# Optimization experiments

Measured on AMD Instinct MI355X. Metric: run time of the kernel, lower is better.

The kernel has to match this reference:

```python
import jax, jax.numpy as jnp
import numpy as np

H = 16
D_MODEL = 1024
D_K = D_MODEL // H
B, S = 8, 1024


def setup_inputs() -> dict:
    key = jax.random.key(0)
    ks = jax.random.split(key, 11)
    scale = 1.0 / np.sqrt(D_MODEL)
    inp = {
        "query": jax.random.normal(ks[0], (B, S, D_MODEL), jnp.float32),
        "key_": jax.random.normal(ks[1], (B, S, D_MODEL), jnp.float32),
        "value": jax.random.normal(ks[2], (B, S, D_MODEL), jnp.float32),
        "w_q": jax.random.normal(ks[3], (D_MODEL, D_MODEL), jnp.float32) * scale,
        "b_q": jnp.zeros((D_MODEL,), jnp.float32),
        "w_k": jax.random.normal(ks[4], (D_MODEL, D_MODEL), jnp.float32) * scale,
        "b_k": jnp.zeros((D_MODEL,), jnp.float32),
        "w_v": jax.random.normal(ks[5], (D_MODEL, D_MODEL), jnp.float32) * scale,
        "b_v": jnp.zeros((D_MODEL,), jnp.float32),
        "w_o": jax.random.normal(ks[6], (D_MODEL, D_MODEL), jnp.float32) * scale,
        "b_o": jnp.zeros((D_MODEL,), jnp.float32),
    }
    return inp


def reference(query, key_, value, w_q, b_q, w_k, b_k, w_v, b_v, w_o, b_o):
    # Linear projections (torch Linear: x @ W.T + b), then split heads: [B,S,D] -> [B,H,S,d_k]
    def proj(x, w, b):
        y = jnp.einsum("bsd,ed->bse", x, w) + b
        return y.reshape(B, S, H, D_K).transpose(0, 2, 1, 3)

    q = proj(query, w_q, b_q)
    k = proj(key_, w_k, b_k)
    v = proj(value, w_v, b_v)

    # Scaled dot-product attention (mask=None, dropout p=0 -> identity)
    scores = jnp.einsum("bhqd,bhkd->bhqk", q, k) / jnp.sqrt(jnp.float32(D_K))
    attn = jax.nn.softmax(scores, axis=-1)
    ctx = jnp.einsum("bhqk,bhkd->bhqd", attn, v)  # [B,H,S,d_k]

    # Merge heads and final output projection
    ctx = ctx.transpose(0, 2, 1, 3).reshape(B, S, D_MODEL)
    return jnp.einsum("bsd,ed->bse", ctx, w_o) + b_o
```

## Files before the change

kernel.cpp:

```cpp
#include <hip/hip_runtime.h>
#include <hip/hip_bf16.h>

#define NH 16
#define DK 64
#define BB 8
#define SS 1024
#define DM 1024
#define MTOT (BB * SS)

typedef float f4v __attribute__((ext_vector_type(4)));
typedef float f16v __attribute__((ext_vector_type(16)));
typedef short s16v8 __attribute__((ext_vector_type(8)));
typedef unsigned short u16v4 __attribute__((ext_vector_type(4)));
typedef unsigned short u16v8 __attribute__((ext_vector_type(8)));

#define EXP2F(x) __builtin_amdgcn_exp2f(x)

__device__ __forceinline__ unsigned short f2bf(float x) {
    unsigned int u = __float_as_uint(x);
    u += 0x7FFFu + ((u >> 16) & 1u);
    return (unsigned short)(u >> 16);
}

__device__ __forceinline__ unsigned int packbf2(float lo, float hi) {
    return ((unsigned int)f2bf(hi) << 16) | f2bf(lo);
}

__device__ __forceinline__ void gload16(const void* g, void* l) {
    __builtin_amdgcn_global_load_lds(
        (const __attribute__((address_space(1))) void*)g,
        (__attribute__((address_space(3))) void*)l, 16, 0, 0);
}

struct Src7 { const float* p[7]; };

__global__ __launch_bounds__(256) void cvt_all(Src7 sp, unsigned short* __restrict__ dst) {
    const size_t e = ((size_t)blockIdx.x * 256 + threadIdx.x) * 8;
    const int unit = (int)(e >> 20);
    int t; size_t base;
    if (unit < 8)       { t = 0; base = 0; }
    else if (unit < 16) { t = 1; base = (size_t)8 << 20; }
    else if (unit < 24) { t = 2; base = (size_t)16 << 20; }
    else                { t = 3 + (unit - 24); base = (size_t)unit << 20; }
    const float* s = sp.p[t] + (e - base);
    f4v a = *(const f4v*)s;
    f4v b = *(const f4v*)(s + 4);
    u16v8 o;
    o[0] = f2bf(a[0]); o[1] = f2bf(a[1]); o[2] = f2bf(a[2]); o[3] = f2bf(a[3]);
    o[4] = f2bf(b[0]); o[5] = f2bf(b[1]); o[6] = f2bf(b[2]); o[7] = f2bf(b[3]);
    *(u16v8*)(dst + e) = o;
}

struct QkvArgs {
    const unsigned short* X[3];
    const unsigned short* W[3];
    const float* bias[3];
    unsigned short* Y[3];
};

__global__ __launch_bounds__(256) void gemm_qkv(QkvArgs a) {
    __shared__ unsigned short As[128 * 32];
    __shared__ unsigned short Bs[128 * 32];
    const int z = blockIdx.z;
    const unsigned short* X = a.X[z];
    const unsigned short* W = a.W[z];
    const float* bias = a.bias[z];
    unsigned short* Y = a.Y[z];

    const int tid = threadIdx.x;
    const int wv = tid >> 6, l = tid & 63;
    const int lq = l & 15, g = l >> 4;
    const int wr = wv >> 1, wc = wv & 1;
    const int m0 = blockIdx.y * 128, n0 = blockIdx.x * 128;

    f4v acc[4][4];
#pragma unroll
    for (int i = 0; i < 4; ++i)
#pragma unroll
        for (int j = 0; j < 4; ++j) acc[i][j] = (f4v){0.f, 0.f, 0.f, 0.f};

    for (int kt = 0; kt < DM / 32; ++kt) {
        const int k0 = kt * 32;
        __syncthreads();
#pragma unroll
        for (int p = 0; p < 2; ++p) {
            const int u = p * 256 + tid;
            const int row = u >> 2, kc = u & 3;
            gload16(X + (size_t)(m0 + row) * DM + k0 + kc * 8, As + (size_t)u * 8);
            gload16(W + (size_t)(n0 + row) * DM + k0 + kc * 8, Bs + (size_t)u * 8);
        }
        __syncthreads();

        s16v8 av[4], bv[4];
#pragma unroll
        for (int i = 0; i < 4; ++i)
            av[i] = *(const s16v8*)(As + (wr * 64 + i * 16 + lq) * 32 + g * 8);
#pragma unroll
        for (int j = 0; j < 4; ++j)
            bv[j] = *(const s16v8*)(Bs + (wc * 64 + j * 16 + lq) * 32 + g * 8);
#pragma unroll
        for (int i = 0; i < 4; ++i)
#pragma unroll
            for (int j = 0; j < 4; ++j)
                acc[i][j] = __builtin_amdgcn_mfma_f32_16x16x32_bf16(av[i], bv[j], acc[i][j], 0, 0, 0);
    }

#pragma unroll
    for (int j = 0; j < 4; ++j) {
        const int col = n0 + wc * 64 + j * 16 + lq;
        const float bvl = bias[col];
#pragma unroll
        for (int i = 0; i < 4; ++i) {
            const int row0 = m0 + wr * 64 + i * 16 + g * 4;
            if (z < 2) {
#pragma unroll
                for (int r = 0; r < 4; ++r) {
                    const int row = row0 + r;
                    const int b_ = row >> 10, s_ = row & (SS - 1);
                    const int h_ = col >> 6, d_ = col & (DK - 1);
                    Y[((size_t)(b_ * NH + h_) * SS + s_) * DK + d_] = f2bf(acc[i][j][r] + bvl);
                }
            } else {
                const int b_ = row0 >> 10, s0_ = row0 & (SS - 1);
                const int h_ = col >> 6, d_ = col & (DK - 1);
                u16v4 o;
#pragma unroll
                for (int r = 0; r < 4; ++r) o[r] = f2bf(acc[i][j][r] + bvl);
                *(u16v4*)&Y[((size_t)(b_ * NH + h_) * DK + d_) * SS + s0_] = o;
            }
        }
    }
}

__global__ __launch_bounds__(256) void gemm_out(const unsigned short* __restrict__ X,
                                                const unsigned short* __restrict__ W,
                                                const float* __restrict__ bias,
                                                float* __restrict__ Y) {
    __shared__ unsigned short As[128 * 32];
    __shared__ unsigned short Bs[128 * 32];
    const int tid = threadIdx.x;
    const int wv = tid >> 6, l = tid & 63;
    const int lq = l & 15, g = l >> 4;
    const int wr = wv >> 1, wc = wv & 1;
    const int m0 = blockIdx.y * 128, n0 = blockIdx.x * 128;

    f4v acc[4][4];
#pragma unroll
    for (int i = 0; i < 4; ++i)
#pragma unroll
        for (int j = 0; j < 4; ++j) acc[i][j] = (f4v){0.f, 0.f, 0.f, 0.f};

    for (int kt = 0; kt < DM / 32; ++kt) {
        const int k0 = kt * 32;
        __syncthreads();
#pragma unroll
        for (int p = 0; p < 2; ++p) {
            const int u = p * 256 + tid;
            const int row = u >> 2, kc = u & 3;
            gload16(X + (size_t)(m0 + row) * DM + k0 + kc * 8, As + (size_t)u * 8);
            gload16(W + (size_t)(n0 + row) * DM + k0 + kc * 8, Bs + (size_t)u * 8);
        }
        __syncthreads();

        s16v8 av[4], bv[4];
#pragma unroll
        for (int i = 0; i < 4; ++i)
            av[i] = *(const s16v8*)(As + (wr * 64 + i * 16 + lq) * 32 + g * 8);
#pragma unroll
        for (int j = 0; j < 4; ++j)
            bv[j] = *(const s16v8*)(Bs + (wc * 64 + j * 16 + lq) * 32 + g * 8);
#pragma unroll
        for (int i = 0; i < 4; ++i)
#pragma unroll
            for (int j = 0; j < 4; ++j)
                acc[i][j] = __builtin_amdgcn_mfma_f32_16x16x32_bf16(av[i], bv[j], acc[i][j], 0, 0, 0);
    }

#pragma unroll
    for (int j = 0; j < 4; ++j) {
        const int col = n0 + wc * 64 + j * 16 + lq;
        const float bvl = bias[col];
#pragma unroll
        for (int i = 0; i < 4; ++i) {
#pragma unroll
            for (int r = 0; r < 4; ++r) {
                const int row = m0 + wr * 64 + i * 16 + g * 4 + r;
                Y[(size_t)row * DM + col] = acc[i][j][r] + bvl;
            }
        }
    }
}

__global__ __launch_bounds__(256) void attn_mfma32(const unsigned short* __restrict__ Qp,
                                                   const unsigned short* __restrict__ Kp,
                                                   const unsigned short* __restrict__ Vt,
                                                   unsigned short* __restrict__ ctx) {
    const int tid = threadIdx.x;
    const int wv = tid >> 6;
    const int l = tid & 63;
    const int l31 = l & 31, hi = l >> 5;
    const int bh = blockIdx.x;
    const int q = blockIdx.y * 128 + wv * 32 + l31;
    const float C = 0.18033688011112042f;

    const unsigned short* Qrow = Qp + ((size_t)bh * SS + q) * DK + hi * 8;
    s16v8 qf[4];
#pragma unroll
    for (int kd = 0; kd < 4; ++kd) qf[kd] = *(const s16v8*)(Qrow + kd * 16);

    const unsigned short* Kb = Kp + (size_t)bh * SS * DK + hi * 8;
    const unsigned short* Vb = Vt + (size_t)bh * DK * SS + hi * 8;

    f16v O0, O1;
#pragma unroll
    for (int r = 0; r < 16; ++r) { O0[r] = 0.f; O1[r] = 0.f; }
    float me = -1e30f;
    float lr = 0.f;

    for (int t = 0; t < SS / 64; ++t) {
        s16v8 kf[2][4];
#pragma unroll
        for (int ks = 0; ks < 2; ++ks)
#pragma unroll
            for (int kd = 0; kd < 4; ++kd)
                kf[ks][kd] = *(const s16v8*)(Kb + (size_t)(t * 64 + ks * 32 + l31) * DK + kd * 16);
        s16v8 vf[2][4];
#pragma unroll
        for (int db = 0; db < 2; ++db)
#pragma unroll
            for (int ksg = 0; ksg < 4; ++ksg)
                vf[db][ksg] = *(const s16v8*)(Vb + (size_t)(db * 32 + l31) * SS + t * 64 + ksg * 16);

        f16v s0, s1;
#pragma unroll
        for (int r = 0; r < 16; ++r) { s0[r] = 0.f; s1[r] = 0.f; }
#pragma unroll
        for (int kd = 0; kd < 4; ++kd) {
            s0 = __builtin_amdgcn_mfma_f32_32x32x16_bf16(kf[0][kd], qf[kd], s0, 0, 0, 0);
            s1 = __builtin_amdgcn_mfma_f32_32x32x16_bf16(kf[1][kd], qf[kd], s1, 0, 0, 0);
        }

        float mx = s0[0];
#pragma unroll
        for (int r = 1; r < 16; ++r) mx = fmaxf(mx, s0[r]);
#pragma unroll
        for (int r = 0; r < 16; ++r) mx = fmaxf(mx, s1[r]);
        mx = fmaxf(mx, __shfl_xor(mx, 32));
        const float mxl = mx * C;

        const bool need = !__all(mxl - me <= 8.0f);
        float corr = 1.0f;
        if (need) {
            const float mnew = fmaxf(me, mxl);
            corr = EXP2F(me - mnew);
            me = mnew;
        }

        float rs = 0.f;
#pragma unroll
        for (int r = 0; r < 16; ++r) { s0[r] = EXP2F(__fmaf_rn(s0[r], C, -me)); rs += s0[r]; }
#pragma unroll
        for (int r = 0; r < 16; ++r) { s1[r] = EXP2F(__fmaf_rn(s1[r], C, -me)); rs += s1[r]; }
        rs += __shfl_xor(rs, 32);
        if (need) {
            lr = lr * corr + rs;
#pragma unroll
            for (int r = 0; r < 16; ++r) { O0[r] *= corr; O1[r] *= corr; }
        } else {
            lr += rs;
        }

        s16v8 pb[2][2];
#pragma unroll
        for (int ks = 0; ks < 2; ++ks) {
            unsigned int u[8], su[8];
#pragma unroll
            for (int i = 0; i < 8; ++i) {
                const float plo = (ks == 0) ? s0[2 * i] : s1[2 * i];
                const float phi = (ks == 0) ? s0[2 * i + 1] : s1[2 * i + 1];
                u[i] = packbf2(plo, phi);
            }
#pragma unroll
            for (int i = 0; i < 8; ++i) su[i] = (unsigned int)__shfl_xor((int)u[i], 32);
#pragma unroll
            for (int kk = 0; kk < 2; ++kk) {
                const int base = 4 * kk + 2 * hi;
                union { unsigned int w[4]; s16v8 s; } f;
                f.w[0] = hi ? su[base] : u[base];
                f.w[1] = hi ? su[base + 1] : u[base + 1];
                f.w[2] = hi ? u[base] : su[base];
                f.w[3] = hi ? u[base + 1] : su[base + 1];
                pb[ks][kk] = f.s;
            }
        }

#pragma unroll
        for (int ksg = 0; ksg < 4; ++ksg) {
            O0 = __builtin_amdgcn_mfma_f32_32x32x16_bf16(vf[0][ksg], pb[ksg >> 1][ksg & 1], O0, 0, 0, 0);
            O1 = __builtin_amdgcn_mfma_f32_32x32x16_bf16(vf[1][ksg], pb[ksg >> 1][ksg & 1], O1, 0, 0, 0);
        }
    }

    const float inv = 1.0f / lr;
    const int b_ = bh >> 4, h_ = bh & 15;
    unsigned short* crow = ctx + ((size_t)b_ * SS + q) * DM + h_ * DK;
#pragma unroll
    for (int g2 = 0; g2 < 4; ++g2) {
        u16v4 o0, o1;
#pragma unroll
        for (int r2 = 0; r2 < 4; ++r2) {
            o0[r2] = f2bf(O0[4 * g2 + r2] * inv);
            o1[r2] = f2bf(O1[4 * g2 + r2] * inv);
        }
        *(u16v4*)(crow + 8 * g2 + 4 * hi) = o0;
        *(u16v4*)(crow + 32 + 8 * g2 + 4 * hi) = o1;
    }
}

extern "C" void kernel_launch(void* const* d_in, const int* in_sizes, int n_in,
                              void* d_out, int out_size, void* d_ws, size_t ws_size,
                              hipStream_t stream) {
    const float* query = (const float*)d_in[0];
    const float* key_  = (const float*)d_in[1];
    const float* value = (const float*)d_in[2];
    const float* w_q = (const float*)d_in[3];
    const float* b_q = (const float*)d_in[4];
    const float* w_k = (const float*)d_in[5];
    const float* b_k = (const float*)d_in[6];
    const float* w_v = (const float*)d_in[7];
    const float* b_v = (const float*)d_in[8];
    const float* w_o = (const float*)d_in[9];
    const float* b_o = (const float*)d_in[10];

    unsigned short* ws = (unsigned short*)d_ws;
    const size_t NX = (size_t)MTOT * DM;
    const size_t NW = (size_t)DM * DM;
    unsigned short* xq  = ws;
    unsigned short* xk  = xq + NX;
    unsigned short* xv  = xk + NX;
    unsigned short* wqb = xv + NX;
    unsigned short* wkb = wqb + NW;
    unsigned short* wvb = wkb + NW;
    unsigned short* wob = wvb + NW;
    unsigned short* Qp  = wob + NW;
    unsigned short* Kp  = Qp + NX;
    unsigned short* VpT = Kp + NX;
    unsigned short* ctx = xq;

    Src7 sp;
    sp.p[0] = query; sp.p[1] = key_; sp.p[2] = value;
    sp.p[3] = w_q; sp.p[4] = w_k; sp.p[5] = w_v; sp.p[6] = w_o;
    cvt_all<<<14336, 256, 0, stream>>>(sp, ws);

    QkvArgs qa;
    qa.X[0] = xq;  qa.X[1] = xk;  qa.X[2] = xv;
    qa.W[0] = wqb; qa.W[1] = wkb; qa.W[2] = wvb;
    qa.bias[0] = b_q; qa.bias[1] = b_k; qa.bias[2] = b_v;
    qa.Y[0] = Qp; qa.Y[1] = Kp; qa.Y[2] = VpT;
    gemm_qkv<<<dim3(DM / 128, MTOT / 128, 3), 256, 0, stream>>>(qa);

    attn_mfma32<<<dim3(BB * NH, SS / 128), 256, 0, stream>>>(Qp, Kp, VpT, ctx);

    gemm_out<<<dim3(DM / 128, MTOT / 128), 256, 0, stream>>>(ctx, wob, b_o, (float*)d_out);
}
```

Measured before the change: 441.0 us.

## Stage K/V tiles through double-buffered LDS via async global-to-LDS loads in attention

The attention kernel now copies each 64-key K tile and V^T tile into shared memory with global_load_lds, double-buffered so the next tile's load overlaps compute on the current one. Each tile is loaded once per workgroup and shared by its four waves, where before every wave read it from global memory itself. The grid is flattened to 1D with bh as the fast index, so workgroups sharing a head are scheduled close together. This adds barriers and a waitcnt per iteration, 32KB of LDS that may limit occupancy, and an extra redundant stage on the last iteration.

```diff
diff --git a/kernel.cpp b/kernel.cpp
--- a/kernel.cpp
+++ b/kernel.cpp
@@ -15,6 +15,7 @@
 typedef unsigned short u16v8 __attribute__((ext_vector_type(8)));
 
 #define EXP2F(x) __builtin_amdgcn_exp2f(x)
+#define WAIT_VM4() __builtin_amdgcn_s_waitcnt(0x0F74)
 
 __device__ __forceinline__ unsigned short f2bf(float x) {
     unsigned int u = __float_as_uint(x);
@@ -195,12 +196,16 @@
                                                    const unsigned short* __restrict__ Kp,
                                                    const unsigned short* __restrict__ Vt,
                                                    unsigned short* __restrict__ ctx) {
+    __shared__ unsigned short Ksh[2][4096];
+    __shared__ unsigned short Vsh[2][4096];
     const int tid = threadIdx.x;
     const int wv = tid >> 6;
     const int l = tid & 63;
     const int l31 = l & 31, hi = l >> 5;
-    const int bh = blockIdx.x;
-    const int q = blockIdx.y * 128 + wv * 32 + l31;
+    const int wgid = blockIdx.x;
+    const int bh = wgid & 127;
+    const int qblk = wgid >> 7;
+    const int q = qblk * 128 + wv * 32 + l31;
     const float C = 0.18033688011112042f;
 
     const unsigned short* Qrow = Qp + ((size_t)bh * SS + q) * DK + hi * 8;
@@ -208,8 +213,19 @@
 #pragma unroll
     for (int kd = 0; kd < 4; ++kd) qf[kd] = *(const s16v8*)(Qrow + kd * 16);
 
-    const unsigned short* Kb = Kp + (size_t)bh * SS * DK + hi * 8;
-    const unsigned short* Vb = Vt + (size_t)bh * DK * SS + hi * 8;
+    const unsigned short* Kb = Kp + (size_t)bh * SS * DK;
+    const unsigned short* Vb = Vt + (size_t)bh * DK * SS;
+
+#define STAGE(buf, t)                                                            \
+    {                                                                            \
+        _Pragma("unroll") for (int p = 0; p < 2; ++p) {                          \
+            const int u = p * 256 + tid;                                         \
+            gload16(Kb + (size_t)((t) * 64 + (u & 63)) * DK + (u >> 6) * 8,      \
+                    &Ksh[buf][(size_t)u * 8]);                                   \
+            gload16(Vb + (size_t)(u & 63) * SS + (t) * 64 + (u >> 6) * 8,        \
+                    &Vsh[buf][(size_t)u * 8]);                                   \
+        }                                                                        \
+    }
 
     f16v O0, O1;
 #pragma unroll
@@ -217,19 +233,27 @@
     float me = -1e30f;
     float lr = 0.f;
 
+    STAGE(0, 0);
+    int cur = 0;
+
     for (int t = 0; t < SS / 64; ++t) {
+        const int tn = (t < SS / 64 - 1) ? t + 1 : t;
+        STAGE(cur ^ 1, tn);
+        WAIT_VM4();
+        __builtin_amdgcn_s_barrier();
+
         s16v8 kf[2][4];
 #pragma unroll
         for (int ks = 0; ks < 2; ++ks)
 #pragma unroll
             for (int kd = 0; kd < 4; ++kd)
-                kf[ks][kd] = *(const s16v8*)(Kb + (size_t)(t * 64 + ks * 32 + l31) * DK + kd * 16);
+                kf[ks][kd] = *(const s16v8*)&Ksh[cur][(((2 * kd + hi) * 64) + ks * 32 + l31) * 8];
         s16v8 vf[2][4];
 #pragma unroll
         for (int db = 0; db < 2; ++db)
 #pragma unroll
             for (int ksg = 0; ksg < 4; ++ksg)
-                vf[db][ksg] = *(const s16v8*)(Vb + (size_t)(db * 32 + l31) * SS + t * 64 + ksg * 16);
+                vf[db][ksg] = *(const s16v8*)&Vsh[cur][(((2 * ksg + hi) * 64) + db * 32 + l31) * 8];
 
         f16v s0, s1;
 #pragma unroll
@@ -299,7 +323,11 @@
             O0 = __builtin_amdgcn_mfma_f32_32x32x16_bf16(vf[0][ksg], pb[ksg >> 1][ksg & 1], O0, 0, 0, 0);
             O1 = __builtin_amdgcn_mfma_f32_32x32x16_bf16(vf[1][ksg], pb[ksg >> 1][ksg & 1], O1, 0, 0, 0);
         }
-    }
+
+        __builtin_amdgcn_s_barrier();
+        cur ^= 1;
+    }
+#undef STAGE
 
     const float inv = 1.0f / lr;
     const int b_ = bh >> 4, h_ = bh & 15;
@@ -359,7 +387,7 @@
     qa.Y[0] = Qp; qa.Y[1] = Kp; qa.Y[2] = VpT;
     gemm_qkv<<<dim3(DM / 128, MTOT / 128, 3), 256, 0, stream>>>(qa);
 
-    attn_mfma32<<<dim3(BB * NH, SS / 128), 256, 0, stream>>>(Qp, Kp, VpT, ctx);
+    attn_mfma32<<<dim3(BB * NH * (SS / 128)), 256, 0, stream>>>(Qp, Kp, VpT, ctx);
 
     gemm_out<<<dim3(DM / 128, MTOT / 128), 256, 0, stream>>>(ctx, wob, b_o, (float*)d_out);
 }
```

New measurement: 394.2 us. 10.6% less time.
